# Kernel optimization log

Measured on AMD Instinct MI355X. Metric: run time of the kernel, lower is better.

The kernel has to match this reference:

```python
import jax, jax.numpy as jnp
import numpy as np

B, N, F_IN, F_HID, F_LAT = 32, 4096, 128, 64, 32


def setup_inputs() -> dict:
    key = jax.random.key(0)
    ks = jax.random.split(key, 7)
    x = jax.random.normal(ks[0], (B, N, F_IN), dtype=jnp.float32)
    q_ids = jax.random.randint(ks[1], (B,), 0, N)
    # dense (soft) adjacency, as stored on the module
    adj = jax.random.uniform(ks[2], (N, N), dtype=jnp.float32)
    W1 = jax.random.normal(ks[3], (F_IN, F_HID), dtype=jnp.float32) * 0.05
    b1 = jax.random.normal(ks[4], (F_HID,), dtype=jnp.float32) * 0.05
    W2 = jax.random.normal(ks[5], (F_HID, F_LAT), dtype=jnp.float32) * 0.05
    b2 = jax.random.normal(ks[6], (F_LAT,), dtype=jnp.float32) * 0.05
    return {"x": x, "q_ids": q_ids, "adj": adj, "W1": W1, "b1": b1, "W2": W2, "b2": b2}


def reference(x, q_ids, adj, W1, b1, W2, b2):
    # Layer 1 (batched, replaces the per-sample python loop):
    # gcn(x, adj) = adj @ (x @ W1) + b1, then relu
    support = jnp.einsum('bnf,fh->bnh', x, W1)          # (B, N, F_HID)
    h = jax.nn.relu(jnp.einsum('nm,bmh->bnh', adj, support) + b1)
    # Layer 2: each sample uses a single row adj[q_id] -> (1, N) aggregation
    rows = adj[q_ids]                                    # (B, N) gather
    agg = jnp.einsum('bn,bnh->bh', rows, h)              # (B, F_HID)
    out = agg @ W2 + b2                                  # (B, F_LAT), squeezed
    return out
```

## Files before the change

### kernel.cpp

```cpp
#include <hip/hip_runtime.h>
#include <hip/hip_bf16.h>
#include <stdint.h>

typedef __attribute__((ext_vector_type(4))) float f32x4;
typedef __attribute__((ext_vector_type(8))) short short8;

#define NN 4096
#define FIN 128
#define FHID 64
#define BATCH 32
#define NJ 2048

__device__ __forceinline__ unsigned short f2bf(float f) {
  unsigned u = __builtin_bit_cast(unsigned, f);
  u = (u + 0x7FFFu + ((u >> 16) & 1u)) >> 16;
  return (unsigned short)u;
}
__device__ __forceinline__ float bf2f(unsigned short h) {
  unsigned u = ((unsigned)h) << 16;
  return __builtin_bit_cast(float, u);
}
__device__ __forceinline__ void gload_lds16(const void* g, void* l) {
  __builtin_amdgcn_global_load_lds(
      (const __attribute__((address_space(1))) unsigned int*)g,
      (__attribute__((address_space(3))) unsigned int*)l, 16, 0, 0);
}

__global__ __launch_bounds__(256) void k_pre(const float* __restrict__ adj,
                                             unsigned short* __restrict__ adjb,
                                             const float* __restrict__ x,
                                             const float* __restrict__ W1,
                                             unsigned short* __restrict__ St) {
  __shared__ unsigned short W1t[FHID * 136];
  __shared__ __align__(16) unsigned short T[FHID * 128];
  const int tid = threadIdx.x;

  if (blockIdx.x >= 1024) {
    long base = ((long)blockIdx.x - 1024) * 2048 + tid;
    const f32x4* in = (const f32x4*)adj;
    f32x4 v[8];
    #pragma unroll
    for (int it = 0; it < 8; ++it) v[it] = in[base + it * 256];
    #pragma unroll
    for (int it = 0; it < 8; ++it) {
      ushort4 o;
      o.x = f2bf(v[it].x); o.y = f2bf(v[it].y);
      o.z = f2bf(v[it].z); o.w = f2bf(v[it].w);
      *(ushort4*)(adjb + (base + it * 256) * 4) = o;
    }
    return;
  }

  for (int i = tid; i < FIN * FHID; i += 256) {
    int f = i >> 6, h = i & 63;
    W1t[h * 136 + f] = f2bf(W1[i]);
  }
  __syncthreads();

  const int bb = blockIdx.x >> 5;
  const int m0 = (blockIdx.x & 31) * 128;
  const int lane = tid & 63, wv = tid >> 6;
  const int fr = lane & 15, fq = lane >> 4;

  short8 bfr[4][4];
  #pragma unroll
  for (int ni = 0; ni < 4; ++ni)
    #pragma unroll
    for (int ks = 0; ks < 4; ++ks)
      bfr[ni][ks] = *(const short8*)&W1t[(ni * 16 + fr) * 136 + ks * 32 + fq * 8];

  const float* xr0 = x + ((size_t)bb * NN + m0 + wv * 32 + fr) * FIN;
  const float* xr1 = xr0 + (size_t)16 * FIN;

  f32x4 z = {0.f, 0.f, 0.f, 0.f};
  f32x4 acc[2][4];
  #pragma unroll
  for (int mf = 0; mf < 2; ++mf)
    #pragma unroll
    for (int ni = 0; ni < 4; ++ni) acc[mf][ni] = z;

  #pragma unroll
  for (int ks = 0; ks < 4; ++ks) {
    #pragma unroll
    for (int mf = 0; mf < 2; ++mf) {
      const float* src = (mf ? xr1 : xr0) + ks * 32 + fq * 8;
      f32x4 lo = *(const f32x4*)src;
      f32x4 hi = *(const f32x4*)(src + 4);
      short8 a;
      #pragma unroll
      for (int j = 0; j < 4; ++j) { a[j] = (short)f2bf(lo[j]); a[4 + j] = (short)f2bf(hi[j]); }
      #pragma unroll
      for (int ni = 0; ni < 4; ++ni)
        acc[mf][ni] = __builtin_amdgcn_mfma_f32_16x16x32_bf16(a, bfr[ni][ks], acc[mf][ni], 0, 0, 0);
    }
  }

  const int cr = (lane >> 4) * 4, cc = lane & 15;
  #pragma unroll
  for (int mf = 0; mf < 2; ++mf)
    #pragma unroll
    for (int ni = 0; ni < 4; ++ni) {
      ushort4 o;
      o.x = f2bf(acc[mf][ni][0]); o.y = f2bf(acc[mf][ni][1]);
      o.z = f2bf(acc[mf][ni][2]); o.w = f2bf(acc[mf][ni][3]);
      *(ushort4*)&T[(ni * 16 + cc) * 128 + wv * 32 + mf * 16 + cr] = o;
    }
  __syncthreads();
  for (int u = tid; u < FHID * 16; u += 256) {
    int row = u >> 4, ch = u & 15;
    *(short8*)(St + (size_t)(bb * FHID + row) * NN + m0 + ch * 8) =
        *(const short8*)&T[row * 128 + ch * 8];
  }
}

#define VMW(N)  asm volatile("s_waitcnt vmcnt(" #N ")" ::: "memory")
#define LGKM0   asm volatile("s_waitcnt lgkmcnt(0)" ::: "memory")
#define BAR     __builtin_amdgcn_s_barrier()

__global__ __launch_bounds__(512, 1) void k_gemm(const unsigned short* __restrict__ A,
                                                 const unsigned short* __restrict__ Bt,
                                                 const float* __restrict__ b1,
                                                 const float* __restrict__ adj,
                                                 const int* __restrict__ q_ids,
                                                 float* __restrict__ partial) {
  __shared__ __align__(16) unsigned short As[2 * 16384];
  __shared__ __align__(16) unsigned short Bs[2 * 8192];
  __shared__ float adjw[2][256];
  __shared__ float red[8][64];

  const int tid  = threadIdx.x;
  const int lane = tid & 63;
  const int wv   = tid >> 6;
  const int wm   = wv >> 1;
  const int wn   = wv & 1;
  const int bm   = blockIdx.x * 256;
  const int bn   = blockIdx.y * 128;
  const int fr   = lane & 15;
  const int fq   = lane >> 4;

  int offA[2][2][2], offB[4][2];
  #pragma unroll
  for (int h = 0; h < 2; ++h)
    #pragma unroll
    for (int m2 = 0; m2 < 2; ++m2) {
      int row = wm * 32 + h * 128 + m2 * 16 + fr;
      #pragma unroll
      for (int ks = 0; ks < 2; ++ks)
        offA[h][m2][ks] = row * 64 + ((((ks << 6) + (fq << 4)) ^ ((row & 7) << 4)) >> 1);
    }
  #pragma unroll
  for (int ni = 0; ni < 4; ++ni) {
    int row = wn * 32 + (ni & 1) * 16 + (ni >> 1) * 64 + fr;
    #pragma unroll
    for (int ks = 0; ks < 2; ++ks)
      offB[ni][ks] = row * 64 + ((((ks << 6) + (fq << 4)) ^ ((row & 7) << 4)) >> 1);
  }

  const int srow = tid >> 3;
  const int scol = ((((tid & 7) << 4) ^ ((srow & 7) << 4)) >> 1);
  const unsigned short* gA00 = A + (size_t)(bm +   0 + srow) * NN + scol;
  const unsigned short* gA01 = A + (size_t)(bm +  64 + srow) * NN + scol;
  const unsigned short* gA10 = A + (size_t)(bm + 128 + srow) * NN + scol;
  const unsigned short* gA11 = A + (size_t)(bm + 192 + srow) * NN + scol;
  const unsigned short* gB0  = Bt + (size_t)(bn +  0 + srow) * NN + scol;
  const unsigned short* gB1  = Bt + (size_t)(bn + 64 + srow) * NN + scol;
  const int ld = tid * 8;

  f32x4 z = {0.f, 0.f, 0.f, 0.f};
  f32x4 acc[4][4];
  #pragma unroll
  for (int i = 0; i < 4; ++i)
    #pragma unroll
    for (int j = 0; j < 4; ++j) acc[i][j] = z;

  short8 av0[2][2], av1[2][2], bvB[2][2], bvA0[2][2], bvA1[2][2];

#define RD_AVA(Ac)                                                             \
    _Pragma("unroll") for (int m2 = 0; m2 < 2; ++m2)                           \
    _Pragma("unroll") for (int ks = 0; ks < 2; ++ks)                           \
      av0[m2][ks] = *(const short8*)((Ac) + offA[0][m2][ks]);
#define RD_AVB(Ac)                                                             \
    _Pragma("unroll") for (int m2 = 0; m2 < 2; ++m2)                           \
    _Pragma("unroll") for (int ks = 0; ks < 2; ++ks)                           \
      av1[m2][ks] = *(const short8*)((Ac) + offA[1][m2][ks]);
#define RD_BV(DST, Bb, P)                                                      \
    _Pragma("unroll") for (int n2 = 0; n2 < 2; ++n2)                           \
    _Pragma("unroll") for (int ks = 0; ks < 2; ++ks)                           \
      DST[n2][ks] = *(const short8*)((Bb) + offB[2 * (P) + n2][ks]);
#define MFMA8(MP, AV, BV, NP)                                                  \
    __builtin_amdgcn_s_setprio(1);                                             \
    _Pragma("unroll") for (int m2 = 0; m2 < 2; ++m2)                           \
    _Pragma("unroll") for (int n2 = 0; n2 < 2; ++n2)                           \
    _Pragma("unroll") for (int ks = 0; ks < 2; ++ks)                           \
      acc[2 * (MP) + m2][2 * (NP) + n2] = __builtin_amdgcn_mfma_f32_16x16x32_bf16( \
          AV[m2][ks], BV[n2][ks], acc[2 * (MP) + m2][2 * (NP) + n2], 0, 0, 0); \
    __builtin_amdgcn_s_setprio(0);

#define TILE(CUR, BVA_C, BVA_N, KQ, DOS, VMWOP) {                              \
    const unsigned short* Ac = As + (CUR) * 16384;                             \
    const unsigned short* Bc = Bs + (CUR) * 8192;                              \
    const unsigned short* Bn = Bs + (1 - (CUR)) * 8192;                        \
                                                                      \
    RD_AVA(Ac)                                                                 \
    RD_BV(bvB, Bc, 1)                                                          \
    if (DOS) {                                                                 \
      gload_lds16(gA00 + (KQ), As + (CUR) * 16384 + 0 * 4096 + ld);            \
      gload_lds16(gA01 + (KQ), As + (CUR) * 16384 + 1 * 4096 + ld);            \
      gload_lds16(gB1  + (KQ), Bs + (CUR) * 8192 + 1 * 4096 + ld);             \
    }                                                                          \
    BAR; LGKM0;                                                                \
    MFMA8(0, av0, BVA_C, 0)                                                    \
    MFMA8(0, av0, bvB, 1)                                                      \
                                                                      \
    RD_AVB(Ac)                                                                 \
    if (DOS) {                                                                 \
      gload_lds16(gA10 + (KQ), As + (CUR) * 16384 + 2 * 4096 + ld);            \
      gload_lds16(gA11 + (KQ), As + (CUR) * 16384 + 3 * 4096 + ld);            \
      gload_lds16(gB0  + (KQ), Bs + (CUR) * 8192 + 0 * 4096 + ld);             \
    }                                                                          \
    VMWOP;                                                                     \
    BAR; LGKM0;                                                                \
    RD_BV(BVA_N, Bn, 0)                                                        \
    MFMA8(1, av1, bvB, 1)                                                      \
    MFMA8(1, av1, BVA_C, 0)                                                    \
  }

  gload_lds16(gB0,       Bs + 0 * 4096 + ld);
  gload_lds16(gB1,       Bs + 1 * 4096 + ld);
  gload_lds16(gA00,      As + 0 * 4096 + ld);
  gload_lds16(gA01,      As + 1 * 4096 + ld);
  gload_lds16(gA10,      As + 2 * 4096 + ld);
  gload_lds16(gA11,      As + 3 * 4096 + ld);
  gload_lds16(gB0  + 64, Bs + 8192 + 0 * 4096 + ld);
  gload_lds16(gB1  + 64, Bs + 8192 + 1 * 4096 + ld);
  gload_lds16(gA00 + 64, As + 16384 + 0 * 4096 + ld);
  gload_lds16(gA01 + 64, As + 16384 + 1 * 4096 + ld);
  gload_lds16(gA10 + 64, As + 16384 + 2 * 4096 + ld);
  gload_lds16(gA11 + 64, As + 16384 + 3 * 4096 + ld);
  VMW(6);
  BAR;
  RD_BV(bvA0, Bs, 0)

  int kq = 128;
  #pragma unroll 1
  for (int g = 0; g < 31; ++g) {
    TILE(0, bvA0, bvA1, kq,      1, VMW(6))
    TILE(1, bvA1, bvA0, kq + 64, 1, VMW(6))
    kq += 128;
  }
  TILE(0, bvA0, bvA1, 0, 0, VMW(0))
  {
    const unsigned short* Ac = As + 16384;
    const unsigned short* Bc = Bs + 8192;
    RD_AVA(Ac)
    RD_BV(bvB, Bc, 1)
    BAR; LGKM0;
    MFMA8(0, av0, bvA1, 0)
    MFMA8(0, av0, bvB, 1)
    RD_AVB(Ac)
    BAR; LGKM0;
    MFMA8(1, av1, bvB, 1)
    MFMA8(1, av1, bvA1, 0)
  }
#undef RD_AVA
#undef RD_AVB
#undef RD_BV
#undef MFMA8
#undef TILE

  const int b0 = bn >> 6;
  {
    int bsel = tid >> 8;
    int rloc = tid & 255;
    adjw[bsel][rloc] = adj[(size_t)q_ids[b0 + bsel] * NN + bm + rloc];
  }
  __syncthreads();

  const int cr = (lane >> 4) * 4;
  const int cc = lane & 15;
  float ps[4];
  #pragma unroll
  for (int ni = 0; ni < 4; ++ni) {
    int colh = wn * 32 + (ni & 1) * 16 + cc;
    float bias = b1[colh];
    float s = 0.f;
    #pragma unroll
    for (int mi = 0; mi < 4; ++mi) {
      int rowl = wm * 32 + (mi & 1) * 16 + (mi >> 1) * 128 + cr;
      #pragma unroll
      for (int r = 0; r < 4; ++r) {
        float v = acc[mi][ni][r] + bias;
        v = v > 0.f ? v : 0.f;
        s += adjw[ni >> 1][rowl + r] * v;
      }
    }
    ps[ni] = s;
  }
  #pragma unroll
  for (int ni = 0; ni < 4; ++ni) {
    ps[ni] += __shfl_xor(ps[ni], 16, 64);
    ps[ni] += __shfl_xor(ps[ni], 32, 64);
  }
  if (lane < 16) {
    #pragma unroll
    for (int ni = 0; ni < 4; ++ni)
      red[wm * 2 + wn][ni * 16 + cc] = ps[ni];
  }
  __syncthreads();
  if (tid < 128) {
    int colLocal = tid;
    int wn2 = (colLocal >> 5) & 1;
    int ni2 = ((colLocal >> 6) << 1) | ((colLocal >> 4) & 1);
    int cc2 = colLocal & 15;
    float s = red[0 + wn2][ni2 * 16 + cc2] + red[2 + wn2][ni2 * 16 + cc2]
            + red[4 + wn2][ni2 * 16 + cc2] + red[6 + wn2][ni2 * 16 + cc2];
    partial[(size_t)blockIdx.x * NJ + bn + colLocal] = s;
  }
}

__global__ __launch_bounds__(1024) void k_out(const float* __restrict__ partial,
                                              const float* __restrict__ W2,
                                              const float* __restrict__ b2,
                                              float* __restrict__ out) {
  __shared__ float aggs[BATCH * FHID];
  int t = threadIdx.x;
  for (int idx = t; idx < BATCH * FHID; idx += 1024) {
    float s = 0.f;
    #pragma unroll
    for (int c = 0; c < 16; ++c) s += partial[c * NJ + idx];
    aggs[idx] = s;
  }
  __syncthreads();
  int b = t >> 5, l = t & 31;
  float o = b2[l];
  #pragma unroll
  for (int h = 0; h < FHID; ++h) o += aggs[b * FHID + h] * W2[h * 32 + l];
  out[b * 32 + l] = o;
}

extern "C" void kernel_launch(void* const* d_in, const int* in_sizes, int n_in,
                              void* d_out, int out_size, void* d_ws, size_t ws_size,
                              hipStream_t stream) {
  const float* x   = (const float*)d_in[0];
  const int*   q   = (const int*)d_in[1];
  const float* adj = (const float*)d_in[2];
  const float* W1  = (const float*)d_in[3];
  const float* b1  = (const float*)d_in[4];
  const float* W2  = (const float*)d_in[5];
  const float* b2  = (const float*)d_in[6];
  float* out = (float*)d_out;

  char* ws = (char*)d_ws;
  unsigned short* adjb   = (unsigned short*)ws;
  unsigned short* St     = (unsigned short*)(ws + (size_t)32 * 1024 * 1024);
  float*          partial= (float*)(ws + (size_t)48 * 1024 * 1024);

  k_pre<<<3072, 256, 0, stream>>>(adj, adjb, x, W1, St);
  dim3 g2(NN / 256, NJ / 128);
  k_gemm<<<g2, 512, 0, stream>>>(adjb, St, b1, adj, q, partial);
  k_out<<<1, 1024, 0, stream>>>(partial, W2, b2, out);
}
```

Measured before the change: 97.35 us.

## Restructure GEMM LDS prefetch schedule to stagger A-half loads across buffers

Reorganizes the double-buffered main loop of the adj@support GEMM so that the second half of the A tile for the next buffer is issued early (into the other buffer), while the first A half and both B halves are reloaded into the current buffer after it is consumed. Both B fragments are now read from the current buffer at tile start instead of carrying the B fragment across tiles in registers, which removes one register array. The prologue, wait counts and epilogue tiles are adjusted accordingly. This aims to spread global-to-LDS traffic more evenly between barriers and hide latency better, at the risk of subtle buffer hazards and changed vmcnt accounting.

```diff
diff --git a/kernel.cpp b/kernel.cpp
--- a/kernel.cpp
+++ b/kernel.cpp
@@ -173,7 +173,7 @@
     #pragma unroll
     for (int j = 0; j < 4; ++j) acc[i][j] = z;
 
-  short8 av0[2][2], av1[2][2], bvB[2][2], bvA0[2][2], bvA1[2][2];
+  short8 av0[2][2], av1[2][2], bv0[2][2], bv1[2][2];
 
 #define RD_AVA(Ac)                                                             \
     _Pragma("unroll") for (int m2 = 0; m2 < 2; ++m2)                           \
@@ -196,72 +196,58 @@
           AV[m2][ks], BV[n2][ks], acc[2 * (MP) + m2][2 * (NP) + n2], 0, 0, 0); \
     __builtin_amdgcn_s_setprio(0);
 
-#define TILE(CUR, BVA_C, BVA_N, KQ, DOS, VMWOP) {                              \
+#define TILE(CUR, KOA, KOB, DOSA, DOSB, VMWA, VMWB) {                          \
     const unsigned short* Ac = As + (CUR) * 16384;                             \
     const unsigned short* Bc = Bs + (CUR) * 8192;                              \
-    const unsigned short* Bn = Bs + (1 - (CUR)) * 8192;                        \
                                                                       \
     RD_AVA(Ac)                                                                 \
-    RD_BV(bvB, Bc, 1)                                                          \
-    if (DOS) {                                                                 \
-      gload_lds16(gA00 + (KQ), As + (CUR) * 16384 + 0 * 4096 + ld);            \
-      gload_lds16(gA01 + (KQ), As + (CUR) * 16384 + 1 * 4096 + ld);            \
-      gload_lds16(gB1  + (KQ), Bs + (CUR) * 8192 + 1 * 4096 + ld);             \
+    RD_BV(bv0, Bc, 0)                                                          \
+    RD_BV(bv1, Bc, 1)                                                          \
+    VMWA;                                                                      \
+    if (DOSA) {         \
+      gload_lds16(gA10 + (KOA), As + (1 - (CUR)) * 16384 + 2 * 4096 + ld);     \
+      gload_lds16(gA11 + (KOA), As + (1 - (CUR)) * 16384 + 3 * 4096 + ld);     \
     }                                                                          \
     BAR; LGKM0;                                                                \
-    MFMA8(0, av0, BVA_C, 0)                                                    \
-    MFMA8(0, av0, bvB, 1)                                                      \
+    MFMA8(0, av0, bv0, 0)                                                      \
+    MFMA8(0, av0, bv1, 1)                                                      \
                                                                       \
     RD_AVB(Ac)                                                                 \
-    if (DOS) {                                                                 \
-      gload_lds16(gA10 + (KQ), As + (CUR) * 16384 + 2 * 4096 + ld);            \
-      gload_lds16(gA11 + (KQ), As + (CUR) * 16384 + 3 * 4096 + ld);            \
-      gload_lds16(gB0  + (KQ), Bs + (CUR) * 8192 + 0 * 4096 + ld);             \
+    VMWB;                                                                      \
+    if (DOSB) {    \
+      gload_lds16(gA00 + (KOB), As + (CUR) * 16384 + 0 * 4096 + ld);           \
+      gload_lds16(gA01 + (KOB), As + (CUR) * 16384 + 1 * 4096 + ld);           \
+      gload_lds16(gB0  + (KOB), Bs + (CUR) * 8192 + 0 * 4096 + ld);            \
+      gload_lds16(gB1  + (KOB), Bs + (CUR) * 8192 + 1 * 4096 + ld);            \
     }                                                                          \
-    VMWOP;                                                                     \
     BAR; LGKM0;                                                                \
-    RD_BV(BVA_N, Bn, 0)                                                        \
-    MFMA8(1, av1, bvB, 1)                                                      \
-    MFMA8(1, av1, BVA_C, 0)                                                    \
-  }
-
+    MFMA8(1, av1, bv1, 1)                                                      \
+    MFMA8(1, av1, bv0, 0)                                                      \
+  }
+
+  gload_lds16(gA00,      As + 0 * 4096 + ld);
+  gload_lds16(gA01,      As + 1 * 4096 + ld);
   gload_lds16(gB0,       Bs + 0 * 4096 + ld);
   gload_lds16(gB1,       Bs + 1 * 4096 + ld);
-  gload_lds16(gA00,      As + 0 * 4096 + ld);
-  gload_lds16(gA01,      As + 1 * 4096 + ld);
   gload_lds16(gA10,      As + 2 * 4096 + ld);
   gload_lds16(gA11,      As + 3 * 4096 + ld);
+  gload_lds16(gA00 + 64, As + 16384 + 0 * 4096 + ld);
+  gload_lds16(gA01 + 64, As + 16384 + 1 * 4096 + ld);
   gload_lds16(gB0  + 64, Bs + 8192 + 0 * 4096 + ld);
   gload_lds16(gB1  + 64, Bs + 8192 + 1 * 4096 + ld);
-  gload_lds16(gA00 + 64, As + 16384 + 0 * 4096 + ld);
-  gload_lds16(gA01 + 64, As + 16384 + 1 * 4096 + ld);
-  gload_lds16(gA10 + 64, As + 16384 + 2 * 4096 + ld);
-  gload_lds16(gA11 + 64, As + 16384 + 3 * 4096 + ld);
-  VMW(6);
+  VMW(4);
   BAR;
-  RD_BV(bvA0, Bs, 0)
-
-  int kq = 128;
+
+  int koa = 64;
+  int kob = 128;
   #pragma unroll 1
   for (int g = 0; g < 31; ++g) {
-    TILE(0, bvA0, bvA1, kq,      1, VMW(6))
-    TILE(1, bvA1, bvA0, kq + 64, 1, VMW(6))
-    kq += 128;
-  }
-  TILE(0, bvA0, bvA1, 0, 0, VMW(0))
-  {
-    const unsigned short* Ac = As + 16384;
-    const unsigned short* Bc = Bs + 8192;
-    RD_AVA(Ac)
-    RD_BV(bvB, Bc, 1)
-    BAR; LGKM0;
-    MFMA8(0, av0, bvA1, 0)
-    MFMA8(0, av0, bvB, 1)
-    RD_AVB(Ac)
-    BAR; LGKM0;
-    MFMA8(1, av1, bvB, 1)
-    MFMA8(1, av1, bvA1, 0)
-  }
+    TILE(0, koa,      kob,      1, 1, VMW(6), VMW(6))
+    TILE(1, koa + 64, kob + 64, 1, 1, VMW(6), VMW(6))
+    koa += 128; kob += 128;
+  }
+  TILE(0, 63 * 64, 0, 1, 0, VMW(6), VMW(6))
+  TILE(1, 0, 0, 0, 0, VMW(2), VMW(0))
 #undef RD_AVA
 #undef RD_AVB
 #undef RD_BV
```

Result: faster. 94.76 us, median of 2 (-2.7%).
